# Performance work log

Hardware: AMD Instinct MI355X
Metric: run time of the kernel (lower is better)

Reference implementation:

```python
import jax, jax.numpy as jnp
import numpy as np

TEMPERATURE = 1.0  # router softmax temperature

def setup_inputs() -> dict:
    key = jax.random.key(0)
    k1, k2, k3 = jax.random.split(key, 3)
    B, C, H, W = 4, 3, 512, 512
    N = 8            # num_branches (original + 7 rain candidates)
    LH, LW = 32, 32  # low-res logit map size
    original = jax.random.normal(k1, (B, C, H, W), dtype=jnp.float32)
    degraded = jax.random.normal(k2, (B, N - 1, C, H, W), dtype=jnp.float32)
    logits = jax.random.normal(k3, (N, LH, LW), dtype=jnp.float32)  # learned low-res routing logits
    return {"original": original, "degraded": degraded, "logits": logits, "topk": 2}


def reference(original, degraded, logits, topk):
    # Candidate stack: [B, N, C, H, W]
    stacked = jnp.concatenate([original[:, None], degraded], axis=1)
    N, LH, LW = logits.shape
    H, W = original.shape[-2:]
    # Bilinear upsample low-res logits (half-pixel centers == torch align_corners=False)
    up = jax.image.resize(logits, (N, H, W), method="bilinear")  # [N, H, W]
    w = jax.nn.softmax(up / TEMPERATURE, axis=0)                 # [N, H, W]
    # Per-pixel top-k gating over branches, then renormalize
    wk = jnp.moveaxis(w, 0, -1)                                  # [H, W, N]
    kth = jax.lax.top_k(wk, topk)[0][..., -1:]                   # [H, W, 1] k-th largest weight
    wk = jnp.where(wk >= kth, wk, 0.0)
    wk = wk / jnp.sum(wk, axis=-1, keepdims=True)
    w = jnp.moveaxis(wk, -1, 0)                                  # [N, H, W]
    # Per-pixel weighted combination across branches -> [B, C, H, W]
    return jnp.einsum("bnchw,nhw->bchw", stacked, w)
```

## Files before the change

kernel.cpp:

```cpp
#include <hip/hip_runtime.h>
#include <math.h>


#define HW_ (512 * 512)

__global__ __launch_bounds__(256) void rain_combine_v2(
    const float* __restrict__ orig,
    const float* __restrict__ deg,
    const float* __restrict__ logits,
    const int* __restrict__ topk_p,
    float* __restrict__ out)
{
    const int g = blockIdx.x * 256 + threadIdx.x;
    const int p0 = g << 1;
    const int h = p0 >> 9;
    const int w0 = p0 & 511;

    const float yc = (h + 0.5f) * 0.0625f - 0.5f;
    const float yf = floorf(yc);
    const float fy = yc - yf;
    const int y0 = (int)yf;
    const int y0c = max(y0, 0), y1c = min(y0 + 1, 31);

    const float xc0 = (w0 + 0.5f) * 0.0625f - 0.5f;
    const float xf = floorf(xc0);
    const int x0 = (int)xf;
    const int x0c = max(x0, 0), x1c = min(x0 + 1, 31);
    const float fx0 = xc0 - xf;
    const float xc1 = (w0 + 1.5f) * 0.0625f - 0.5f;
    const float fx1 = xc1 - xf;

    const int o00 = y0c * 32 + x0c;
    const int o01 = y0c * 32 + x1c;
    const int o10 = y1c * 32 + x0c;
    const int o11 = y1c * 32 + x1c;

    const float A00 = (1.f - fy) * (1.f - fx0), A01 = (1.f - fy) * fx0;
    const float A10 = fy * (1.f - fx0),         A11 = fy * fx0;
    const float B00 = (1.f - fy) * (1.f - fx1), B01 = (1.f - fy) * fx1;
    const float B10 = fy * (1.f - fx1),         B11 = fy * fx1;

    float u[2][8];
    #pragma unroll
    for (int n = 0; n < 8; ++n) {
        const float* Lb = logits + n * 1024;
        const float t00 = Lb[o00], t01 = Lb[o01], t10 = Lb[o10], t11 = Lb[o11];
        u[0][n] = A00 * t00 + A01 * t01 + A10 * t10 + A11 * t11;
        u[1][n] = B00 * t00 + B01 * t01 + B10 * t10 + B11 * t11;
    }

    const int k = *topk_p;

    float wf[2][8];
    #pragma unroll
    for (int i = 0; i < 2; ++i) {
        float mx = u[i][0];
        #pragma unroll
        for (int n = 1; n < 8; ++n) mx = fmaxf(mx, u[i][n]);
        float e[8];
        float s = 0.f;
        #pragma unroll
        for (int n = 0; n < 8; ++n) { e[n] = expf(u[i][n] - mx); s += e[n]; }
        float wg[8];
        #pragma unroll
        for (int n = 0; n < 8; ++n) wg[n] = e[n] / s;

        float kth = -INFINITY;
        #pragma unroll
        for (int n = 0; n < 8; ++n) {
            int gt = 0, ge = 0;
            #pragma unroll
            for (int j = 0; j < 8; ++j) {
                gt += (wg[j] >  wg[n]);
                ge += (wg[j] >= wg[n]);
            }
            if (gt < k && ge >= k) kth = wg[n];
        }

        float S = 0.f;
        #pragma unroll
        for (int n = 0; n < 8; ++n) if (wg[n] >= kth) S += wg[n];
        #pragma unroll
        for (int n = 0; n < 8; ++n) wf[i][n] = (wg[n] >= kth) ? (wg[n] / S) : 0.f;
    }

    float acc[24];
    #pragma unroll
    for (int i = 0; i < 24; ++i) acc[i] = 0.f;

    #pragma unroll
    for (int n = 0; n < 8; ++n) {
        const bool need = (wf[0][n] != 0.f) || (wf[1][n] != 0.f);
        if (need) {
            const float w0n = wf[0][n], w1n = wf[1][n];
            const float* base = (n == 0) ? (orig + p0)
                                         : (deg + (size_t)(n - 1) * 3 * HW_ + p0);
            const int bstr = (n == 0) ? 3 * HW_ : 21 * HW_;
            #pragma unroll
            for (int b = 0; b < 4; ++b) {
                #pragma unroll
                for (int c = 0; c < 3; ++c) {
                    const float2 v = *reinterpret_cast<const float2*>(
                        base + (size_t)b * bstr + (size_t)c * HW_);
                    acc[(b * 3 + c) * 2 + 0] += w0n * v.x;
                    acc[(b * 3 + c) * 2 + 1] += w1n * v.y;
                }
            }
        }
    }

    #pragma unroll
    for (int b = 0; b < 4; ++b) {
        #pragma unroll
        for (int c = 0; c < 3; ++c) {
            float2 o;
            o.x = acc[(b * 3 + c) * 2 + 0];
            o.y = acc[(b * 3 + c) * 2 + 1];
            *reinterpret_cast<float2*>(out + (size_t)(b * 3 + c) * HW_ + p0) = o;
        }
    }
}

extern "C" void kernel_launch(void* const* d_in, const int* in_sizes, int n_in,
                              void* d_out, int out_size, void* d_ws, size_t ws_size,
                              hipStream_t stream) {
    const float* orig   = (const float*)d_in[0];
    const float* deg    = (const float*)d_in[1];
    const float* logits = (const float*)d_in[2];
    const int*   topk   = (const int*)d_in[3];
    float* out = (float*)d_out;

    const int groups = (512 * 512) / 2;
    rain_combine_v2<<<dim3(groups / 256), dim3(256), 0, stream>>>(
        orig, deg, logits, topk, out);
}
```

Before: 145.0 us.

## Split batch across grid y-dimension and drop softmax normalization before top-k

Adds a batch grid dimension so each thread handles one batch image instead of all four, giving four times as many threads and fewer accumulators per thread. Routing weights are now recomputed per batch, which duplicates that work fourfold. Top-k selection and renormalization now run on unnormalized exponentials, removing the softmax divide and using a single reciprocal. The workload is memory-bound (roughly 100MB read), so the added parallelism mainly helps by keeping more loads in flight.

```diff
diff --git a/kernel.cpp b/kernel.cpp
--- a/kernel.cpp
+++ b/kernel.cpp
@@ -4,16 +4,17 @@
 
 #define HW_ (512 * 512)
 
-__global__ __launch_bounds__(256) void rain_combine_v2(
+__global__ __launch_bounds__(256) void rain_combine_v3(
     const float* __restrict__ orig,
     const float* __restrict__ deg,
     const float* __restrict__ logits,
     const int* __restrict__ topk_p,
     float* __restrict__ out)
 {
-    const int g = blockIdx.x * 256 + threadIdx.x;
+    const int g  = blockIdx.x * 256 + threadIdx.x;
+    const int b  = blockIdx.y;
     const int p0 = g << 1;
-    const int h = p0 >> 9;
+    const int h  = p0 >> 9;
     const int w0 = p0 & 511;
 
     const float yc = (h + 0.5f) * 0.0625f - 0.5f;
@@ -27,8 +28,7 @@
     const int x0 = (int)xf;
     const int x0c = max(x0, 0), x1c = min(x0 + 1, 31);
     const float fx0 = xc0 - xf;
-    const float xc1 = (w0 + 1.5f) * 0.0625f - 0.5f;
-    const float fx1 = xc1 - xf;
+    const float fx1 = fx0 + 0.0625f;
 
     const int o00 = y0c * 32 + x0c;
     const int o01 = y0c * 32 + x1c;
@@ -58,12 +58,8 @@
         #pragma unroll
         for (int n = 1; n < 8; ++n) mx = fmaxf(mx, u[i][n]);
         float e[8];
-        float s = 0.f;
         #pragma unroll
-        for (int n = 0; n < 8; ++n) { e[n] = expf(u[i][n] - mx); s += e[n]; }
-        float wg[8];
-        #pragma unroll
-        for (int n = 0; n < 8; ++n) wg[n] = e[n] / s;
+        for (int n = 0; n < 8; ++n) e[n] = expf(u[i][n] - mx);
 
         float kth = -INFINITY;
         #pragma unroll
@@ -71,53 +67,48 @@
             int gt = 0, ge = 0;
             #pragma unroll
             for (int j = 0; j < 8; ++j) {
-                gt += (wg[j] >  wg[n]);
-                ge += (wg[j] >= wg[n]);
+                gt += (e[j] >  e[n]);
+                ge += (e[j] >= e[n]);
             }
-            if (gt < k && ge >= k) kth = wg[n];
+            if (gt < k && ge >= k) kth = e[n];
         }
 
         float S = 0.f;
         #pragma unroll
-        for (int n = 0; n < 8; ++n) if (wg[n] >= kth) S += wg[n];
+        for (int n = 0; n < 8; ++n) if (e[n] >= kth) S += e[n];
+        const float rS = 1.f / S;
         #pragma unroll
-        for (int n = 0; n < 8; ++n) wf[i][n] = (wg[n] >= kth) ? (wg[n] / S) : 0.f;
+        for (int n = 0; n < 8; ++n) wf[i][n] = (e[n] >= kth) ? (e[n] * rS) : 0.f;
     }
 
-    float acc[24];
+    float acc[6];
     #pragma unroll
-    for (int i = 0; i < 24; ++i) acc[i] = 0.f;
+    for (int i = 0; i < 6; ++i) acc[i] = 0.f;
 
     #pragma unroll
     for (int n = 0; n < 8; ++n) {
         const bool need = (wf[0][n] != 0.f) || (wf[1][n] != 0.f);
         if (need) {
             const float w0n = wf[0][n], w1n = wf[1][n];
-            const float* base = (n == 0) ? (orig + p0)
-                                         : (deg + (size_t)(n - 1) * 3 * HW_ + p0);
-            const int bstr = (n == 0) ? 3 * HW_ : 21 * HW_;
+            const float* base = (n == 0)
+                ? (orig + (size_t)b * 3 * HW_ + p0)
+                : (deg + ((size_t)b * 21 + (size_t)(n - 1) * 3) * HW_ + p0);
             #pragma unroll
-            for (int b = 0; b < 4; ++b) {
-                #pragma unroll
-                for (int c = 0; c < 3; ++c) {
-                    const float2 v = *reinterpret_cast<const float2*>(
-                        base + (size_t)b * bstr + (size_t)c * HW_);
-                    acc[(b * 3 + c) * 2 + 0] += w0n * v.x;
-                    acc[(b * 3 + c) * 2 + 1] += w1n * v.y;
-                }
+            for (int c = 0; c < 3; ++c) {
+                const float2 v = *reinterpret_cast<const float2*>(base + (size_t)c * HW_);
+                acc[c * 2 + 0] += w0n * v.x;
+                acc[c * 2 + 1] += w1n * v.y;
             }
         }
     }
 
+    float* ob = out + (size_t)b * 3 * HW_ + p0;
     #pragma unroll
-    for (int b = 0; b < 4; ++b) {
-        #pragma unroll
-        for (int c = 0; c < 3; ++c) {
-            float2 o;
-            o.x = acc[(b * 3 + c) * 2 + 0];
-            o.y = acc[(b * 3 + c) * 2 + 1];
-            *reinterpret_cast<float2*>(out + (size_t)(b * 3 + c) * HW_ + p0) = o;
-        }
+    for (int c = 0; c < 3; ++c) {
+        float2 o;
+        o.x = acc[c * 2 + 0];
+        o.y = acc[c * 2 + 1];
+        *reinterpret_cast<float2*>(ob + (size_t)c * HW_) = o;
     }
 }
 
@@ -130,7 +121,7 @@
     const int*   topk   = (const int*)d_in[3];
     float* out = (float*)d_out;
 
-    const int groups = (512 * 512) / 2;
-    rain_combine_v2<<<dim3(groups / 256), dim3(256), 0, stream>>>(
+    const int pairs = (512 * 512) / 2;
+    rain_combine_v3<<<dim3(pairs / 256, 4), dim3(256), 0, stream>>>(
         orig, deg, logits, topk, out);
 }
```

Result: no change. 143.5 us (-1.1%).
